# Optimization experiments

Measured on AMD Instinct MI355X. Metric: run time of the kernel, lower is better.

The kernel has to match this reference:

```python
import jax, jax.numpy as jnp
import numpy as np

FEATURES_DIM = 100000
NUM_FIELDS = 39
EMBED_DIM = 64
DIM_INT = (2, 3)
RANK = (32, 32)
BATCH = 8192


def setup_inputs() -> dict:
    key = jax.random.key(0)
    ks = jax.random.split(key, 6)
    x = jax.random.randint(ks[0], (BATCH, NUM_FIELDS), 0, FEATURES_DIM)
    embed_table = jax.random.normal(ks[1], (FEATURES_DIM, EMBED_DIM), dtype=jnp.float32) * 0.01
    linear_w = jax.random.normal(ks[2], (FEATURES_DIM, 1), dtype=jnp.float32) * 0.01
    linear_bias = jnp.zeros((1,), dtype=jnp.float32)
    # trunc_normal_(std=0.01) approximated by clipped normal
    W0 = jnp.clip(jax.random.normal(ks[3], (DIM_INT[0], RANK[0], NUM_FIELDS), dtype=jnp.float32) * 0.01, -0.02, 0.02)
    W1 = jnp.clip(jax.random.normal(ks[4], (DIM_INT[1], RANK[1], NUM_FIELDS), dtype=jnp.float32) * 0.01, -0.02, 0.02)
    return {"x": x, "embed_table": embed_table, "linear_w": linear_w,
            "linear_bias": linear_bias, "W0": W0, "W1": W1}


def _calc_cross(W, emb):
    # W: (l, j, k) = (dim_int, rank, num_fields); emb: (b, k, i) = (batch, fields, embed)
    # dot_products[b,i,j,l] = sum_k W[l,j,k] * emb[b,k,i]
    dp = jnp.einsum('ljk,bki->bijl', W, emb)          # (b, embed, rank, dim_int)
    prod_over_l = jnp.prod(dp, axis=3)                # (b, embed, rank)
    return jnp.sum(prod_over_l, axis=(1, 2))          # (b,)


def reference(x, embed_table, linear_w, linear_bias, W0, W1):
    emb = embed_table[x]                              # (b, fields, embed)
    lin = jnp.sum(linear_w[x], axis=1) + linear_bias  # (b, 1)
    ret = lin[:, 0] + _calc_cross(W0, emb) + _calc_cross(W1, emb)
    return ret                                        # (b,)
```

## Files before the change

kernel.cpp:

```cpp
#include <hip/hip_runtime.h>
#include <hip/hip_bf16.h>

#define BATCH    8192
#define NF       39
#define ED       64
#define RANK     32
#define KST      72
#define NFRAG    15

typedef _Float16 half8  __attribute__((ext_vector_type(8)));
typedef float    f32x16 __attribute__((ext_vector_type(16)));

__global__ void prep_w(const float* __restrict__ W0,
                       const float* __restrict__ W1,
                       half8* __restrict__ wsW) {
    int d = blockIdx.x * 256 + threadIdx.x;
    if (d >= NFRAG * 64) return;
    int fid  = d >> 6;
    int lane = d & 63;
    int l = fid / 3, kc = fid % 3;
    int j = lane & 31, kh = lane >> 5;
    const float* base = (l < 2) ? (W0 + (l * RANK + j) * NF)
                                : (W1 + ((l - 2) * RANK + j) * NF);
    half8 h;
#pragma unroll
    for (int e = 0; e < 8; ++e) {
        int k = kc * 16 + kh * 8 + e;
        h[e] = (k < NF) ? (_Float16)base[k] : (_Float16)0.0f;
    }
    wsW[d] = h;
}

__global__ __launch_bounds__(256, 3) void tfm_kernel(
    const int*   __restrict__ x,
    const float* __restrict__ embed,
    const float* __restrict__ linw,
    const float* __restrict__ lbias,
    const half8* __restrict__ wsW,
    float*       __restrict__ out)
{
    __shared__ __align__(16) _Float16 Ws[NFRAG * 64 * 8];
    __shared__ __align__(16) _Float16 Ef[4][ED][KST];

    const int t    = threadIdx.x;
    const int lane = t & 63;
    const int w    = t >> 6;
    const int s    = blockIdx.x * 4 + w;

    const int j  = lane & 31;
    const int kh = lane >> 5;

    const int xi_v = (lane < NF) ? x[s * NF + lane] : 0;
    const float lv = (lane < NF) ? linw[xi_v] : 0.0f;

    float r[NF];
#pragma unroll
    for (int k = 0; k < NF; ++k) {
        int xi = __builtin_amdgcn_readlane(xi_v, k);
        r[k] = embed[(size_t)xi * ED + lane];
    }

    {
        const uint4* src = (const uint4*)wsW;
        uint4*       dst = (uint4*)Ws;
#pragma unroll
        for (int i = 0; i < NFRAG * 64 / 256; ++i)
            dst[i * 256 + t] = src[i * 256 + t];
        if (t < NFRAG * 64 - 768) dst[768 + t] = src[768 + t];
    }

    const float bias = lbias[0];

#pragma unroll
    for (int c6 = 0; c6 < 6; ++c6) {
        half8 hh;
#pragma unroll
        for (int e = 0; e < 8; ++e) {
            int k = c6 * 8 + e;
            hh[e] = (k < NF) ? (_Float16)r[k] : (_Float16)0.0f;
        }
        *(half8*)&Ef[w][lane][c6 * 8] = hh;
    }

    __syncthreads();

    const half8* Wf = (const half8*)Ws;
    float ssum = lv;

#pragma unroll
    for (int tile = 0; tile < 2; ++tile) {
        const int c = tile * 32 + j;
        half8 bf[3];
#pragma unroll
        for (int kc = 0; kc < 3; ++kc)
            bf[kc] = *(const half8*)&Ef[w][c][kc * 16 + kh * 8];

        {
            f32x16 a0, a1;
#pragma unroll
            for (int e = 0; e < 16; ++e) { a0[e] = 0.0f; a1[e] = 0.0f; }
#pragma unroll
            for (int kc = 0; kc < 3; ++kc) {
                a0 = __builtin_amdgcn_mfma_f32_32x32x16_f16(Wf[(0 * 3 + kc) * 64 + lane], bf[kc], a0, 0, 0, 0);
                a1 = __builtin_amdgcn_mfma_f32_32x32x16_f16(Wf[(1 * 3 + kc) * 64 + lane], bf[kc], a1, 0, 0, 0);
            }
#pragma unroll
            for (int e = 0; e < 16; ++e) ssum += a0[e] * a1[e];
        }
        {
            f32x16 c0, c1, c2;
#pragma unroll
            for (int e = 0; e < 16; ++e) { c0[e] = 0.0f; c1[e] = 0.0f; c2[e] = 0.0f; }
#pragma unroll
            for (int kc = 0; kc < 3; ++kc) {
                c0 = __builtin_amdgcn_mfma_f32_32x32x16_f16(Wf[(2 * 3 + kc) * 64 + lane], bf[kc], c0, 0, 0, 0);
                c1 = __builtin_amdgcn_mfma_f32_32x32x16_f16(Wf[(3 * 3 + kc) * 64 + lane], bf[kc], c1, 0, 0, 0);
                c2 = __builtin_amdgcn_mfma_f32_32x32x16_f16(Wf[(4 * 3 + kc) * 64 + lane], bf[kc], c2, 0, 0, 0);
            }
#pragma unroll
            for (int e = 0; e < 16; ++e) ssum += c0[e] * c1[e] * c2[e];
        }
    }

#pragma unroll
    for (int off = 32; off > 0; off >>= 1) ssum += __shfl_down(ssum, off, 64);
    if (lane == 0) out[s] = ssum + bias;
}

extern "C" void kernel_launch(void* const* d_in, const int* in_sizes, int n_in,
                              void* d_out, int out_size, void* d_ws, size_t ws_size,
                              hipStream_t stream) {
    const int*   x     = (const int*)  d_in[0];
    const float* embed = (const float*)d_in[1];
    const float* linw  = (const float*)d_in[2];
    const float* lbias = (const float*)d_in[3];
    const float* W0    = (const float*)d_in[4];
    const float* W1    = (const float*)d_in[5];
    float*       out   = (float*)d_out;
    half8*       wsW   = (half8*)d_ws;

    prep_w<<<(NFRAG * 64 + 255) / 256, 256, 0, stream>>>(W0, W1, wsW);
    tfm_kernel<<<BATCH / 4, 256, 0, stream>>>(x, embed, linw, lbias, wsW, out);
}
```

Baseline: 94.98 us.

## Gather embeddings with float4 loads into transposed LDS tile, raise occupancy

Replaces per-lane scalar embedding gathers (39 scalar loads per lane, one row element each) with 10 float4 loads per lane, where 16 lanes cover a 64-float row and four rows are fetched per instruction. The data is converted to fp16 and stored into a field-major transposed LDS buffer with padded stride, and pad rows 39..47 are zeroed explicitly. MFMA B-fragments are then assembled from eight strided 16-bit LDS reads instead of one 16-byte vector read. Launch bounds raise the waves-per-SIMD target from 3 to 4, which cuts register pressure and the large r[39] array. The cost is more, smaller LDS reads and possible bank conflicts on the fragment build.

New measurement: 113.8 us. 19.8% more time.

```diff
diff --git a/kernel.cpp b/kernel.cpp
--- a/kernel.cpp
+++ b/kernel.cpp
@@ -5,9 +5,11 @@
 #define NF       39
 #define ED       64
 #define RANK     32
-#define KST      72
 #define NFRAG    15
+#define KROWS    48
+#define KSTH     66
 
+typedef _Float16 half2  __attribute__((ext_vector_type(2)));
 typedef _Float16 half8  __attribute__((ext_vector_type(8)));
 typedef float    f32x16 __attribute__((ext_vector_type(16)));
 
@@ -31,7 +33,7 @@
     wsW[d] = h;
 }
 
-__global__ __launch_bounds__(256, 3) void tfm_kernel(
+__global__ __launch_bounds__(256, 4) void tfm_kernel(
     const int*   __restrict__ x,
     const float* __restrict__ embed,
     const float* __restrict__ linw,
@@ -40,25 +42,20 @@
     float*       __restrict__ out)
 {
     __shared__ __align__(16) _Float16 Ws[NFRAG * 64 * 8];
-    __shared__ __align__(16) _Float16 Ef[4][ED][KST];
+    __shared__ __align__(4)  _Float16 EfT[4][KROWS][KSTH];
 
     const int t    = threadIdx.x;
     const int lane = t & 63;
     const int w    = t >> 6;
     const int s    = blockIdx.x * 4 + w;
 
-    const int j  = lane & 31;
-    const int kh = lane >> 5;
+    const int sub = lane & 15;
+    const int g   = lane >> 4;
+    const int j   = lane & 31;
+    const int kh  = lane >> 5;
 
     const int xi_v = (lane < NF) ? x[s * NF + lane] : 0;
     const float lv = (lane < NF) ? linw[xi_v] : 0.0f;
-
-    float r[NF];
-#pragma unroll
-    for (int k = 0; k < NF; ++k) {
-        int xi = __builtin_amdgcn_readlane(xi_v, k);
-        r[k] = embed[(size_t)xi * ED + lane];
-    }
 
     {
         const uint4* src = (const uint4*)wsW;
@@ -69,19 +66,31 @@
         if (t < NFRAG * 64 - 768) dst[768 + t] = src[768 + t];
     }
 
-    const float bias = lbias[0];
+    float4 gv[10];
+#pragma unroll
+    for (int q = 0; q < 10; ++q) {
+        int kq = q * 4 + g;
+        int xi = __shfl(xi_v, kq, 64);
+        gv[q] = *(const float4*)(embed + (size_t)xi * ED + sub * 4);
+    }
 
 #pragma unroll
-    for (int c6 = 0; c6 < 6; ++c6) {
-        half8 hh;
-#pragma unroll
-        for (int e = 0; e < 8; ++e) {
-            int k = c6 * 8 + e;
-            hh[e] = (k < NF) ? (_Float16)r[k] : (_Float16)0.0f;
-        }
-        *(half8*)&Ef[w][lane][c6 * 8] = hh;
+    for (int q = 0; q < 10; ++q) {
+        int kq = q * 4 + g;
+        half2 h01; h01[0] = (_Float16)gv[q].x; h01[1] = (_Float16)gv[q].y;
+        half2 h23; h23[0] = (_Float16)gv[q].z; h23[1] = (_Float16)gv[q].w;
+        *(half2*)&EfT[w][kq][sub * 4 + 0] = h01;
+        *(half2*)&EfT[w][kq][sub * 4 + 2] = h23;
     }
 
+    if (lane < 33) {
+        half2 z; z[0] = (_Float16)0.0f; z[1] = (_Float16)0.0f;
+#pragma unroll
+        for (int rr = 39; rr < KROWS; ++rr)
+            *(half2*)&EfT[w][rr][lane * 2] = z;
+    }
+
+    const float bias = lbias[0];
     __syncthreads();
 
     const half8* Wf = (const half8*)Ws;
@@ -90,10 +99,13 @@
 #pragma unroll
     for (int tile = 0; tile < 2; ++tile) {
         const int c = tile * 32 + j;
+
         half8 bf[3];
 #pragma unroll
         for (int kc = 0; kc < 3; ++kc)
-            bf[kc] = *(const half8*)&Ef[w][c][kc * 16 + kh * 8];
+#pragma unroll
+            for (int e = 0; e < 8; ++e)
+                bf[kc][e] = EfT[w][kc * 16 + kh * 8 + e][c];
 
         {
             f32x16 a0, a1;
```

## Process four samples per wave with double-buffered embedding gathers

Applied to the files above, without the earlier changes.

Each wave now handles four samples instead of one, and the grid shrinks to match. The embedding gathers for the next sample are issued into a second register buffer while the current sample is packed into LDS and run through MFMA, so gather latency overlaps compute. This also spreads the per-block cost of copying the W fragments into LDS over four times as many samples. The cost is more registers for the two 39-float buffers under launch_bounds(256,3), a possible spill risk, and only 512 blocks, which reduces parallelism across CUs.

New measurement: 121.4 us. 1.28x slower.

```diff
diff --git a/kernel.cpp b/kernel.cpp
--- a/kernel.cpp
+++ b/kernel.cpp
@@ -7,6 +7,7 @@
 #define RANK     32
 #define KST      72
 #define NFRAG    15
+#define SPW      4
 
 typedef _Float16 half8  __attribute__((ext_vector_type(8)));
 typedef float    f32x16 __attribute__((ext_vector_type(16)));
@@ -45,20 +46,19 @@
     const int t    = threadIdx.x;
     const int lane = t & 63;
     const int w    = t >> 6;
-    const int s    = blockIdx.x * 4 + w;
+    const int s0   = (blockIdx.x * 4 + w) * SPW;
 
     const int j  = lane & 31;
     const int kh = lane >> 5;
 
-    const int xi_v = (lane < NF) ? x[s * NF + lane] : 0;
-    const float lv = (lane < NF) ? linw[xi_v] : 0.0f;
-
-    float r[NF];
+    int xv[SPW];
 #pragma unroll
-    for (int k = 0; k < NF; ++k) {
-        int xi = __builtin_amdgcn_readlane(xi_v, k);
-        r[k] = embed[(size_t)xi * ED + lane];
-    }
+    for (int si = 0; si < SPW; ++si)
+        xv[si] = (lane < NF) ? x[(s0 + si) * NF + lane] : 0;
+    float lv[SPW];
+#pragma unroll
+    for (int si = 0; si < SPW; ++si)
+        lv[si] = (lane < NF) ? linw[xv[si]] : 0.0f;
 
     {
         const uint4* src = (const uint4*)wsW;
@@ -68,63 +68,78 @@
             dst[i * 256 + t] = src[i * 256 + t];
         if (t < NFRAG * 64 - 768) dst[768 + t] = src[768 + t];
     }
-
     const float bias = lbias[0];
 
+    float r0[NF], r1[NF];
+
+    auto issue = [&](int si, float* dst) {
 #pragma unroll
-    for (int c6 = 0; c6 < 6; ++c6) {
-        half8 hh;
+        for (int k = 0; k < NF; ++k) {
+            int xi = __builtin_amdgcn_readlane(xv[si], k);
+            dst[k] = embed[(size_t)xi * ED + lane];
+        }
+    };
+    auto pack = [&](const float* src) {
 #pragma unroll
-        for (int e = 0; e < 8; ++e) {
-            int k = c6 * 8 + e;
-            hh[e] = (k < NF) ? (_Float16)r[k] : (_Float16)0.0f;
+        for (int c6 = 0; c6 < 6; ++c6) {
+            half8 hh;
+#pragma unroll
+            for (int e = 0; e < 8; ++e) {
+                int k = c6 * 8 + e;
+                hh[e] = (k < NF) ? (_Float16)src[k] : (_Float16)0.0f;
+            }
+            *(half8*)&Ef[w][lane][c6 * 8] = hh;
         }
-        *(half8*)&Ef[w][lane][c6 * 8] = hh;
-    }
+    };
+    const half8* Wf = (const half8*)Ws;
+    auto compute_store = [&](float lvv, int sidx) {
+        float ssum = lvv;
+#pragma unroll
+        for (int tile = 0; tile < 2; ++tile) {
+            const int c = tile * 32 + j;
+            half8 bf[3];
+#pragma unroll
+            for (int kc = 0; kc < 3; ++kc)
+                bf[kc] = *(const half8*)&Ef[w][c][kc * 16 + kh * 8];
+            {
+                f32x16 a0, a1;
+#pragma unroll
+                for (int e = 0; e < 16; ++e) { a0[e] = 0.0f; a1[e] = 0.0f; }
+#pragma unroll
+                for (int kc = 0; kc < 3; ++kc) {
+                    a0 = __builtin_amdgcn_mfma_f32_32x32x16_f16(Wf[(0 * 3 + kc) * 64 + lane], bf[kc], a0, 0, 0, 0);
+                    a1 = __builtin_amdgcn_mfma_f32_32x32x16_f16(Wf[(1 * 3 + kc) * 64 + lane], bf[kc], a1, 0, 0, 0);
+                }
+#pragma unroll
+                for (int e = 0; e < 16; ++e) ssum += a0[e] * a1[e];
+            }
+            {
+                f32x16 c0, c1, c2;
+#pragma unroll
+                for (int e = 0; e < 16; ++e) { c0[e] = 0.0f; c1[e] = 0.0f; c2[e] = 0.0f; }
+#pragma unroll
+                for (int kc = 0; kc < 3; ++kc) {
+                    c0 = __builtin_amdgcn_mfma_f32_32x32x16_f16(Wf[(2 * 3 + kc) * 64 + lane], bf[kc], c0, 0, 0, 0);
+                    c1 = __builtin_amdgcn_mfma_f32_32x32x16_f16(Wf[(3 * 3 + kc) * 64 + lane], bf[kc], c1, 0, 0, 0);
+                    c2 = __builtin_amdgcn_mfma_f32_32x32x16_f16(Wf[(4 * 3 + kc) * 64 + lane], bf[kc], c2, 0, 0, 0);
+                }
+#pragma unroll
+                for (int e = 0; e < 16; ++e) ssum += c0[e] * c1[e] * c2[e];
+            }
+        }
+#pragma unroll
+        for (int off = 32; off > 0; off >>= 1) ssum += __shfl_down(ssum, off, 64);
+        if (lane == 0) out[sidx] = ssum + bias;
+    };
 
+    issue(0, r0);
+    issue(1, r1);
     __syncthreads();
 
-    const half8* Wf = (const half8*)Ws;
-    float ssum = lv;
-
-#pragma unroll
-    for (int tile = 0; tile < 2; ++tile) {
-        const int c = tile * 32 + j;
-        half8 bf[3];
-#pragma unroll
-        for (int kc = 0; kc < 3; ++kc)
-            bf[kc] = *(const half8*)&Ef[w][c][kc * 16 + kh * 8];
-
-        {
-            f32x16 a0, a1;
-#pragma unroll
-            for (int e = 0; e < 16; ++e) { a0[e] = 0.0f; a1[e] = 0.0f; }
-#pragma unroll
-            for (int kc = 0; kc < 3; ++kc) {
-                a0 = __builtin_amdgcn_mfma_f32_32x32x16_f16(Wf[(0 * 3 + kc) * 64 + lane], bf[kc], a0, 0, 0, 0);
-                a1 = __builtin_amdgcn_mfma_f32_32x32x16_f16(Wf[(1 * 3 + kc) * 64 + lane], bf[kc], a1, 0, 0, 0);
-            }
-#pragma unroll
-            for (int e = 0; e < 16; ++e) ssum += a0[e] * a1[e];
-        }
-        {
-            f32x16 c0, c1, c2;
-#pragma unroll
-            for (int e = 0; e < 16; ++e) { c0[e] = 0.0f; c1[e] = 0.0f; c2[e] = 0.0f; }
-#pragma unroll
-            for (int kc = 0; kc < 3; ++kc) {
-                c0 = __builtin_amdgcn_mfma_f32_32x32x16_f16(Wf[(2 * 3 + kc) * 64 + lane], bf[kc], c0, 0, 0, 0);
-                c1 = __builtin_amdgcn_mfma_f32_32x32x16_f16(Wf[(3 * 3 + kc) * 64 + lane], bf[kc], c1, 0, 0, 0);
-                c2 = __builtin_amdgcn_mfma_f32_32x32x16_f16(Wf[(4 * 3 + kc) * 64 + lane], bf[kc], c2, 0, 0, 0);
-            }
-#pragma unroll
-            for (int e = 0; e < 16; ++e) ssum += c0[e] * c1[e] * c2[e];
-        }
-    }
-
-#pragma unroll
-    for (int off = 32; off > 0; off >>= 1) ssum += __shfl_down(ssum, off, 64);
-    if (lane == 0) out[s] = ssum + bias;
+    pack(r0); issue(2, r0); compute_store(lv[0], s0 + 0);
+    pack(r1); issue(3, r1); compute_store(lv[1], s0 + 1);
+    pack(r0);               compute_store(lv[2], s0 + 2);
+    pack(r1);               compute_store(lv[3], s0 + 3);
 }
 
 extern "C" void kernel_launch(void* const* d_in, const int* in_sizes, int n_in,
@@ -140,5 +155,5 @@
     half8*       wsW   = (half8*)d_ws;
 
     prep_w<<<(NFRAG * 64 + 255) / 256, 256, 0, stream>>>(W0, W1, wsW);
-    tfm_kernel<<<BATCH / 4, 256, 0, stream>>>(x, embed, linw, lbias, wsW, out);
+    tfm_kernel<<<BATCH / (4 * SPW), 256, 0, stream>>>(x, embed, linw, lbias, wsW, out);
 }
```
